# Optimization experiments

Hardware: AMD Instinct MI355X
Metric: run time of the kernel (lower is better)

Reference implementation:

```python
import jax, jax.numpy as jnp
import numpy as np

B, INPLANES, H, W = 32, 1024, 14, 14
PLANES, WIDTH, OUTC = 256, 256, 1024   # width = planes*(base_width/64)*groups; OUTC = planes*4
BITS = (2, 4, 8)                        # bit_list -> lv = 2**bit per expert
GN_GROUPS = 4
EPS = 1e-5


def _qact(x, lv):
    # quantized ReLU (PACT-style, clip [0,1], lv uniform levels) with STE
    y = jnp.clip(x, 0.0, 1.0)
    q = jnp.round(y * (lv - 1)) / (lv - 1)
    return y + jax.lax.stop_gradient(q - y)


def _qw(w, lv):
    # symmetric per-tensor weight quantization with STE
    n = lv // 2 - 1
    if n < 1:
        n = 1
    s = jnp.max(jnp.abs(w)) + 1e-12
    q = jnp.round(w / s * n) / n * s
    return w + jax.lax.stop_gradient(q - w)


def _conv(x, w, stride=1, pad=0):
    return jax.lax.conv_general_dilated(
        x, w, (stride, stride), [(pad, pad), (pad, pad)],
        dimension_numbers=('NCHW', 'OIHW', 'NCHW'))


def _bn(x, g, b, m, v):
    # inference-mode BatchNorm2d with running stats
    inv = g / jnp.sqrt(v + EPS)
    return x * inv[:, None, None] + (b - m * inv)[:, None, None]


def _expert(x, lv, w1, w2, w3, bn1, bn2):
    # quantized Bottleneck expert: qrelu -> conv1x1 -> bn -> relu -> qrelu -> conv3x3 -> bn -> relu -> qrelu -> conv1x1
    h = _conv(_qact(x, lv), _qw(w1, lv))
    h = jax.nn.relu(_bn(h, *bn1))
    h = _conv(_qact(h, lv), _qw(w2, lv), stride=1, pad=1)
    h = jax.nn.relu(_bn(h, *bn2))
    return _conv(_qact(h, lv), _qw(w3, lv))


def setup_inputs() -> dict:
    key = jax.random.key(0)
    ks = jax.random.split(key, 16)
    return {
        'x': jax.random.normal(ks[0], (B, INPLANES, H, W), jnp.float32),
        'mask': jax.random.randint(ks[1], (B,), 0, len(BITS), jnp.int32),
        'w1': jax.random.normal(ks[2], (WIDTH, INPLANES, 1, 1), jnp.float32) * 0.03,
        'w2': jax.random.normal(ks[3], (WIDTH, WIDTH, 3, 3), jnp.float32) * 0.03,
        'w3': jax.random.normal(ks[4], (OUTC, WIDTH, 1, 1), jnp.float32) * 0.03,
        'bn1_g': jax.random.uniform(ks[5], (WIDTH,), jnp.float32, 0.5, 1.5),
        'bn1_b': jax.random.normal(ks[6], (WIDTH,), jnp.float32) * 0.1,
        'bn1_m': jax.random.normal(ks[7], (WIDTH,), jnp.float32) * 0.1,
        'bn1_v': jax.random.uniform(ks[8], (WIDTH,), jnp.float32, 0.5, 1.5),
        'bn2_g': jax.random.uniform(ks[9], (WIDTH,), jnp.float32, 0.5, 1.5),
        'bn2_b': jax.random.normal(ks[10], (WIDTH,), jnp.float32) * 0.1,
        'bn2_m': jax.random.normal(ks[11], (WIDTH,), jnp.float32) * 0.1,
        'bn2_v': jax.random.uniform(ks[12], (WIDTH,), jnp.float32, 0.5, 1.5),
        'gn_g': jax.random.uniform(ks[13], (OUTC,), jnp.float32, 0.5, 1.5),
        'gn_b': jax.random.normal(ks[14], (OUTC,), jnp.float32) * 0.1,
    }


def reference(x, mask, w1, w2, w3, bn1_g, bn1_b, bn1_m, bn1_v,
              bn2_g, bn2_b, bn2_m, bn2_v, gn_g, gn_b):
    bn1 = (bn1_g, bn1_b, bn1_m, bn1_v)
    bn2 = (bn2_g, bn2_b, bn2_m, bn2_v)
    # sparse MoE: per-sample mask selects one quantized expert; combine masked outputs
    out = jnp.zeros((x.shape[0], OUTC, x.shape[2], x.shape[3]), x.dtype)
    for e, bit in enumerate(BITS):
        sel = (mask == e).astype(x.dtype)[:, None, None, None]
        out = out + sel * _expert(x, 2 ** bit, w1, w2, w3, bn1, bn2)
    # GroupNorm(4, OUTC)
    b_, c_, h_, w_ = out.shape
    g = out.reshape(b_, GN_GROUPS, c_ // GN_GROUPS, h_, w_)
    mu = g.mean(axis=(2, 3, 4), keepdims=True)
    var = g.var(axis=(2, 3, 4), keepdims=True)
    g = (g - mu) / jnp.sqrt(var + EPS)
    out = g.reshape(b_, c_, h_, w_) * gn_g[:, None, None] + gn_b[:, None, None]
    # residual (downsample=None, inplanes == planes*expansion) + relu
    return jax.nn.relu(out + x)
```

## Files before the change

kernel.cpp:

```cpp
#include <hip/hip_runtime.h>
#include <hip/hip_bf16.h>

typedef __attribute__((ext_vector_type(8))) short short8;
typedef __attribute__((ext_vector_type(4))) float f32x4;

#define PIX  196
#define EPSN 1e-5f

#define BO_XQ   256
#define BO_W2Q  BO_XQ
#define BO_W3Q  (BO_XQ + 3538944)
#define BO_H1Q  (BO_XQ + 12845056)
#define BO_H2Q  (BO_H1Q + 3211264)
#define BO_W1Q  (BO_H2Q + 3211264)
#define BO_GNS  (BO_W1Q + 1572864)
#define BO_PMAX (BO_GNS + 8192)

__device__ __forceinline__ float e_ascale(int e) { return e == 0 ? 3.f : (e == 1 ? 15.f : 255.f); }
__device__ __forceinline__ float e_nq(int e)     { return e == 0 ? 1.f : (e == 1 ? 7.f : 127.f); }

__device__ __forceinline__ f32x4 mfma16(short8 a, short8 b, f32x4 c) {
    return __builtin_amdgcn_mfma_f32_16x16x32_bf16(a, b, c, 0, 0, 0);
}
__device__ __forceinline__ float wmax_reduce(const char* wsb, int t) {
    const float* pm = (const float*)(wsb + BO_PMAX) + t * 48;
    float s = 0.f;
    #pragma unroll
    for (int k = 0; k < 48; ++k) s = fmaxf(s, pm[k]);
    return s + 1e-12f;
}

__global__ __launch_bounds__(256) void maxabs_kernel(
        const float* __restrict__ w1, const float* __restrict__ w2,
        const float* __restrict__ w3, float* __restrict__ pmax) {
    int t = blockIdx.y;
    const float* w = t == 0 ? w1 : (t == 1 ? w2 : w3);
    int n = (t == 1) ? 256 * 256 * 9 : 256 * 1024;
    float m = 0.f;
    for (int i = blockIdx.x * 256 + threadIdx.x; i < n; i += 48 * 256)
        m = fmaxf(m, fabsf(w[i]));
    __shared__ float red[256];
    red[threadIdx.x] = m;
    __syncthreads();
    for (int s = 128; s > 0; s >>= 1) {
        if (threadIdx.x < s) red[threadIdx.x] = fmaxf(red[threadIdx.x], red[threadIdx.x + s]);
        __syncthreads();
    }
    if (threadIdx.x == 0) pmax[t * 48 + blockIdx.x] = red[0];
}

__global__ __launch_bounds__(256) void prep_w1x(
        const float* __restrict__ w1, const float* __restrict__ x,
        const int* __restrict__ mask, char* wsb) {
    __shared__ float xs[64][197];
    if (blockIdx.x < 1024) {
        int idx = blockIdx.x * 256 + threadIdx.x;
        float s = wmax_reduce(wsb, 0);
        float v = w1[idx];
        __hip_bfloat16* dst = (__hip_bfloat16*)(wsb + BO_W1Q);
        #pragma unroll
        for (int e = 0; e < 3; ++e)
            dst[e * 262144 + idx] = __float2bfloat16(rintf(v / s * e_nq(e)));
    } else {
        int bx = blockIdx.x - 1024;
        int b = bx >> 4, c0 = (bx & 15) * 64;
        float ascale = e_ascale(mask[b]);
        int tid = threadIdx.x;
        for (int idx = tid; idx < 64 * 196; idx += 256) {
            int ci = idx / 196, p = idx - ci * 196;
            xs[ci][p] = x[((size_t)b * 1024 + c0 + ci) * 196 + p];
        }
        __syncthreads();
        __hip_bfloat16* xq = (__hip_bfloat16*)(wsb + BO_XQ);
        for (int idx = tid; idx < 196 * 64; idx += 256) {
            int p = idx / 64, ci = idx - p * 64;
            float v = fminf(fmaxf(xs[ci][p], 0.f), 1.f);
            xq[((size_t)b * 196 + p) * 1024 + c0 + ci] = __float2bfloat16(rintf(v * ascale));
        }
    }
}

__global__ __launch_bounds__(256) void prepw23_kernel(
        const float* __restrict__ w2, const float* __restrict__ w3, char* wsb) {
    int idx = blockIdx.x * 256 + threadIdx.x;
    if (idx < 589824) {
        float s = wmax_reduce(wsb, 1);
        float v = w2[idx];
        int co = idx / 2304, r = idx - co * 2304, ci = r / 9, tap = r - ci * 9;
        __hip_bfloat16* dst = (__hip_bfloat16*)(wsb + BO_W2Q);
        size_t off = ((size_t)tap * 256 + co) * 256 + ci;
        #pragma unroll
        for (int e = 0; e < 3; ++e)
            dst[e * 589824 + off] = __float2bfloat16(rintf(v / s * e_nq(e)));
    } else {
        int i2 = idx - 589824;
        float s = wmax_reduce(wsb, 2);
        float v = w3[i2];
        __hip_bfloat16* dst = (__hip_bfloat16*)(wsb + BO_W3Q);
        #pragma unroll
        for (int e = 0; e < 3; ++e)
            dst[e * 262144 + i2] = __float2bfloat16(rintf(v / s * e_nq(e)));
    }
}

__global__ __launch_bounds__(256) void conv1_mfma(
        char* wsb, const int* __restrict__ mask,
        const float* __restrict__ bg, const float* __restrict__ bb,
        const float* __restrict__ bm, const float* __restrict__ bv) {
    int b = blockIdx.z;
    int e = mask[b];
    float ascale = e_ascale(e);
    float s1 = wmax_reduce(wsb, 0);
    float kscale = (s1 / e_nq(e)) / ascale;

    const short* xq  = (const short*)(wsb + BO_XQ) + (size_t)b * 196 * 1024;
    const short* w1q = (const short*)(wsb + BO_W1Q) + (size_t)e * 256 * 1024;
    __hip_bfloat16* h1q = (__hip_bfloat16*)(wsb + BO_H1Q) + (size_t)b * 196 * 256;

    __shared__ short As[64 * 136];
    __shared__ short Bs[128 * 136];

    int tid = threadIdx.x, w = tid >> 6, lane = tid & 63, r15 = lane & 15, g = lane >> 4;
    int px0 = blockIdx.x * 56, coB = blockIdx.y * 128;

    short8 ra[4], rb[8];
    auto load_tile = [&](int t) {
        int k0 = t * 128;
        #pragma unroll
        for (int ii = 0; ii < 4; ++ii) {
            int idx = ii * 256 + tid;
            int arow = idx >> 4, ac = (idx & 15) * 8;
            ra[ii] = *(const short8*)(xq + (size_t)min(px0 + arow, 195) * 1024 + k0 + ac);
        }
        #pragma unroll
        for (int ii = 0; ii < 8; ++ii) {
            int idx = ii * 256 + tid;
            int brow = idx >> 4, bc = (idx & 15) * 8;
            rb[ii] = *(const short8*)(w1q + (size_t)(coB + brow) * 1024 + k0 + bc);
        }
    };
    auto store_tile = [&]() {
        #pragma unroll
        for (int ii = 0; ii < 4; ++ii) {
            int idx = ii * 256 + tid;
            *(short8*)(As + (idx >> 4) * 136 + (idx & 15) * 8) = ra[ii];
        }
        #pragma unroll
        for (int ii = 0; ii < 8; ++ii) {
            int idx = ii * 256 + tid;
            *(short8*)(Bs + (idx >> 4) * 136 + (idx & 15) * 8) = rb[ii];
        }
    };

    f32x4 acc[4][2] = {};
    load_tile(0);
    for (int t = 0; t < 8; ++t) {
        __syncthreads();
        store_tile();
        __syncthreads();
        if (t < 7) load_tile(t + 1);
        #pragma unroll
        for (int ks = 0; ks < 4; ++ks) {
            short8 bf0 = *(const short8*)(Bs + (w * 32 + r15) * 136 + ks * 32 + g * 8);
            short8 bf1 = *(const short8*)(Bs + (w * 32 + 16 + r15) * 136 + ks * 32 + g * 8);
            #pragma unroll
            for (int m = 0; m < 4; ++m) {
                short8 af = *(const short8*)(As + (m * 16 + r15) * 136 + ks * 32 + g * 8);
                acc[m][0] = mfma16(af, bf0, acc[m][0]);
                acc[m][1] = mfma16(af, bf1, acc[m][1]);
            }
        }
    }
    #pragma unroll
    for (int n = 0; n < 2; ++n) {
        int co = coB + w * 32 + n * 16 + r15;
        float inv = bg[co] * rsqrtf(bv[co] + EPSN);
        float mm = kscale * inv;
        float beta = bb[co] - bm[co] * inv;
        #pragma unroll
        for (int m = 0; m < 4; ++m)
            #pragma unroll
            for (int r = 0; r < 4; ++r) {
                int s = m * 16 + g * 4 + r, px = px0 + s;
                if (s < 56 && px < 196) {
                    float h = fmaxf(acc[m][n][r] * mm + beta, 0.f);
                    h1q[(size_t)px * 256 + co] = __float2bfloat16(rintf(fminf(h, 1.f) * ascale));
                }
            }
    }
}

__global__ __launch_bounds__(256) void conv2_mfma(
        char* wsb, const int* __restrict__ mask,
        const float* __restrict__ bg, const float* __restrict__ bb,
        const float* __restrict__ bm, const float* __restrict__ bv) {
    int b = blockIdx.z;
    int e = mask[b];
    float ascale = e_ascale(e);
    float s2 = wmax_reduce(wsb, 1);
    float kscale = (s2 / e_nq(e)) / ascale;

    const short* h1q = (const short*)(wsb + BO_H1Q) + (size_t)b * 196 * 256;
    const short* w2q = (const short*)(wsb + BO_W2Q) + (size_t)e * 589824;
    __hip_bfloat16* h2q = (__hip_bfloat16*)(wsb + BO_H2Q) + (size_t)b * 196 * 256;

    __shared__ short Xs[6 * 16 * 40];
    __shared__ short Ws9[9 * 64 * 40];

    int tid = threadIdx.x, w = tid >> 6, lane = tid & 63, r15 = lane & 15, g = lane >> 4;
    int r0 = blockIdx.x * 4;
    int px0 = blockIdx.x * 56;
    int coB = blockIdx.y * 64;
    const short8 z8 = {0, 0, 0, 0, 0, 0, 0, 0};

    int wco = tid >> 2, wc8 = (tid & 3) * 8;

    int rr[4], cc[4];
    #pragma unroll
    for (int m = 0; m < 4; ++m) {
        int s0 = min(m * 16 + r15, 55);
        rr[m] = s0 / 14; cc[m] = s0 - rr[m] * 14;
    }

    short8 rx[2], rw[9];
    auto load_tile = [&](int sl) {
        int ci0 = sl * 32;
        #pragma unroll
        for (int ii = 0; ii < 2; ++ii) {
            int idx = ii * 256 + tid;
            rx[ii] = z8;
            if (idx < 384) {
                int xc = idx & 3, xsx = (idx >> 2) & 15, xsy = idx >> 6;
                int iy = r0 - 1 + xsy, ix = xsx - 1;
                if ((unsigned)iy < 14u && (unsigned)ix < 14u)
                    rx[ii] = *(const short8*)(h1q + (size_t)(iy * 14 + ix) * 256 + ci0 + xc * 8);
            }
        }
        #pragma unroll
        for (int tap = 0; tap < 9; ++tap)
            rw[tap] = *(const short8*)(w2q + ((size_t)tap * 256 + coB + wco) * 256 + ci0 + wc8);
    };
    auto store_tile = [&]() {
        #pragma unroll
        for (int ii = 0; ii < 2; ++ii) {
            int idx = ii * 256 + tid;
            if (idx < 384) {
                int xc = idx & 3, xsx = (idx >> 2) & 15, xsy = idx >> 6;
                *(short8*)(Xs + (xsy * 16 + xsx) * 40 + xc * 8) = rx[ii];
            }
        }
        #pragma unroll
        for (int tap = 0; tap < 9; ++tap)
            *(short8*)(Ws9 + (tap * 64 + wco) * 40 + wc8) = rw[tap];
    };

    f32x4 acc[4] = {};
    load_tile(0);
    for (int sl = 0; sl < 8; ++sl) {
        __syncthreads();
        store_tile();
        __syncthreads();
        if (sl < 7) load_tile(sl + 1);
        #pragma unroll
        for (int tap = 0; tap < 9; ++tap) {
            int ty = tap / 3, tx = tap - ty * 3;
            short8 bf = *(const short8*)(Ws9 + (tap * 64 + w * 16 + r15) * 40 + g * 8);
            #pragma unroll
            for (int m = 0; m < 4; ++m) {
                short8 af = *(const short8*)(Xs + ((rr[m] + ty) * 16 + cc[m] + tx) * 40 + g * 8);
                acc[m] = mfma16(af, bf, acc[m]);
            }
        }
    }
    int co = coB + w * 16 + r15;
    float inv = bg[co] * rsqrtf(bv[co] + EPSN);
    float mm = kscale * inv;
    float beta = bb[co] - bm[co] * inv;
    #pragma unroll
    for (int m = 0; m < 4; ++m)
        #pragma unroll
        for (int r = 0; r < 4; ++r) {
            int s = m * 16 + g * 4 + r, px = px0 + s;
            if (s < 56 && px < 196) {
                float h = fmaxf(acc[m][r] * mm + beta, 0.f);
                h2q[(size_t)px * 256 + co] = __float2bfloat16(rintf(fminf(h, 1.f) * ascale));
            }
        }
}

__global__ __launch_bounds__(256) void conv3_mfma(
        char* wsb, const int* __restrict__ mask, float* __restrict__ out) {
    int b = blockIdx.z;
    int e = mask[b];
    float ascale = e_ascale(e);
    float s3 = wmax_reduce(wsb, 2);
    float kscale = (s3 / e_nq(e)) / ascale;

    const short* h2q = (const short*)(wsb + BO_H2Q) + (size_t)b * 196 * 256;
    const short* w3q = (const short*)(wsb + BO_W3Q) + (size_t)e * 1024 * 256;
    float* ob = out + (size_t)b * 1024 * 196;

    __shared__ float Ct[128 * 58];
    __shared__ float rs[256], rss[256];
    short* As = (short*)Ct;
    short* Bs = As + 64 * 72;

    int tid = threadIdx.x, w = tid >> 6, lane = tid & 63, r15 = lane & 15, g = lane >> 4;
    int px0 = blockIdx.x * 56;
    int coQ = blockIdx.y * 128;
    int gslot = (b * 4 + (blockIdx.y >> 1)) * 8 + (blockIdx.y & 1) * 4 + blockIdx.x;

    short8 ra[2], rb[4];
    auto load_tile = [&](int t) {
        int k0 = t * 64;
        #pragma unroll
        for (int ii = 0; ii < 2; ++ii) {
            int idx = ii * 256 + tid;
            int arow = idx >> 3, ac = (idx & 7) * 8;
            ra[ii] = *(const short8*)(h2q + (size_t)min(px0 + arow, 195) * 256 + k0 + ac);
        }
        #pragma unroll
        for (int ii = 0; ii < 4; ++ii) {
            int idx = ii * 256 + tid;
            int brow = idx >> 3, bc = (idx & 7) * 8;
            rb[ii] = *(const short8*)(w3q + (size_t)(coQ + brow) * 256 + k0 + bc);
        }
    };
    auto store_tile = [&]() {
        #pragma unroll
        for (int ii = 0; ii < 2; ++ii) {
            int idx = ii * 256 + tid;
            *(short8*)(As + (idx >> 3) * 72 + (idx & 7) * 8) = ra[ii];
        }
        #pragma unroll
        for (int ii = 0; ii < 4; ++ii) {
            int idx = ii * 256 + tid;
            *(short8*)(Bs + (idx >> 3) * 72 + (idx & 7) * 8) = rb[ii];
        }
    };

    f32x4 acc[4][2] = {};
    load_tile(0);
    for (int t = 0; t < 4; ++t) {
        __syncthreads();
        store_tile();
        __syncthreads();
        if (t < 3) load_tile(t + 1);
        #pragma unroll
        for (int ks = 0; ks < 2; ++ks) {
            short8 bf0 = *(const short8*)(Bs + (w * 32 + r15) * 72 + ks * 32 + g * 8);
            short8 bf1 = *(const short8*)(Bs + (w * 32 + 16 + r15) * 72 + ks * 32 + g * 8);
            #pragma unroll
            for (int m = 0; m < 4; ++m) {
                short8 af = *(const short8*)(As + (m * 16 + r15) * 72 + ks * 32 + g * 8);
                acc[m][0] = mfma16(af, bf0, acc[m][0]);
                acc[m][1] = mfma16(af, bf1, acc[m][1]);
            }
        }
    }
    __syncthreads();
    #pragma unroll
    for (int n = 0; n < 2; ++n)
        #pragma unroll
        for (int m = 0; m < 4; ++m)
            #pragma unroll
            for (int r = 0; r < 4; ++r) {
                int s = m * 16 + g * 4 + r;
                if (s < 56) Ct[(w * 32 + n * 16 + r15) * 58 + s] = acc[m][n][r];
            }
    __syncthreads();
    float sum = 0.f, ss = 0.f;
    for (int idx = tid; idx < 128 * 56; idx += 256) {
        int col = idx / 56, s = idx - col * 56, px = px0 + s;
        if (px < 196) {
            float v = Ct[col * 58 + s] * kscale;
            ob[(size_t)(coQ + col) * 196 + px] = v;
            sum += v; ss += v * v;
        }
    }
    rs[tid] = sum; rss[tid] = ss;
    __syncthreads();
    for (int st = 128; st > 0; st >>= 1) {
        if (tid < st) { rs[tid] += rs[tid + st]; rss[tid] += rss[tid + st]; }
        __syncthreads();
    }
    if (tid == 0) {
        float* gns = (float*)(wsb + BO_GNS);
        gns[gslot * 2] = rs[0];
        gns[gslot * 2 + 1] = rss[0];
    }
}

__global__ __launch_bounds__(256) void gn_apply(
        float* __restrict__ out, const float* __restrict__ x,
        const float* __restrict__ gg, const float* __restrict__ gb, const char* wsb) {
    int bgid = blockIdx.x >> 4, six = blockIdx.x & 15;
    int g = bgid & 3;
    const float* gns = (const float*)(wsb + BO_GNS);
    float s = 0.f, q = 0.f;
    #pragma unroll
    for (int k = 0; k < 8; ++k) { s += gns[(bgid * 8 + k) * 2]; q += gns[(bgid * 8 + k) * 2 + 1]; }
    float mu = s * (1.f / 50176.f);
    float var = q * (1.f / 50176.f) - mu * mu;
    float rstd = rsqrtf(var + EPSN);

    size_t base = (size_t)bgid * 50176 + six * 3136;
    float4* po = (float4*)(out + base);
    const float4* px4 = (const float4*)(x + base);
    int tid = threadIdx.x;
    for (int i = tid; i < 784; i += 256) {
        int off = six * 3136 + i * 4;
        int gc = g * 256 + off / 196;
        float sc = gg[gc] * rstd;
        float sh = gb[gc] - mu * sc;
        float4 v = po[i], xv = px4[i];
        v.x = fmaxf(v.x * sc + sh + xv.x, 0.f);
        v.y = fmaxf(v.y * sc + sh + xv.y, 0.f);
        v.z = fmaxf(v.z * sc + sh + xv.z, 0.f);
        v.w = fmaxf(v.w * sc + sh + xv.w, 0.f);
        po[i] = v;
    }
}

extern "C" void kernel_launch(void* const* d_in, const int* in_sizes, int n_in,
                              void* d_out, int out_size, void* d_ws, size_t ws_size,
                              hipStream_t stream) {
    (void)in_sizes; (void)n_in; (void)out_size; (void)ws_size;
    const float* x    = (const float*)d_in[0];
    const int*   mask = (const int*)d_in[1];
    const float* w1   = (const float*)d_in[2];
    const float* w2   = (const float*)d_in[3];
    const float* w3   = (const float*)d_in[4];
    const float* b1g  = (const float*)d_in[5];
    const float* b1b  = (const float*)d_in[6];
    const float* b1m  = (const float*)d_in[7];
    const float* b1v  = (const float*)d_in[8];
    const float* b2g  = (const float*)d_in[9];
    const float* b2b  = (const float*)d_in[10];
    const float* b2m  = (const float*)d_in[11];
    const float* b2v  = (const float*)d_in[12];
    const float* gng  = (const float*)d_in[13];
    const float* gnb  = (const float*)d_in[14];
    char* wsb = (char*)d_ws;
    float* out = (float*)d_out;

    maxabs_kernel<<<dim3(48, 3), 256, 0, stream>>>(w1, w2, w3, (float*)(wsb + BO_PMAX));
    prep_w1x<<<1536, 256, 0, stream>>>(w1, x, mask, wsb);
    conv1_mfma<<<dim3(4, 2, 32), 256, 0, stream>>>(wsb, mask, b1g, b1b, b1m, b1v);
    prepw23_kernel<<<3328, 256, 0, stream>>>(w2, w3, wsb);
    conv2_mfma<<<dim3(4, 4, 32), 256, 0, stream>>>(wsb, mask, b2g, b2b, b2m, b2v);
    conv3_mfma<<<dim3(4, 8, 32), 256, 0, stream>>>(wsb, mask, out);
    gn_apply<<<2048, 256, 0, stream>>>(out, x, gng, gnb, wsb);
}
```

Before: 101.6 us.

## Quantize w1/w3 on the fly in GEMMs, merge prep kernels, shrink conv tiles

The max-abs reduction now runs inside the same launch as activation quantization, which removes one kernel launch. The separate pre-quantized w1 and w3 buffers are dropped, and conv1 and conv3 now read fp32 weights and quantize them while loading tiles. conv1 and conv2 switch to smaller output tiles (64 and 32 channels) with a 2x2 wave split, which doubles their grid size to raise occupancy and parallelism. The cost is redundant per-block weight quantization and more fp32 weight traffic in the GEMMs, and conv1 now runs twice as many K iterations with smaller tiles.

```diff
diff --git a/kernel.cpp b/kernel.cpp
--- a/kernel.cpp
+++ b/kernel.cpp
@@ -9,11 +9,9 @@
 
 #define BO_XQ   256
 #define BO_W2Q  BO_XQ
-#define BO_W3Q  (BO_XQ + 3538944)
 #define BO_H1Q  (BO_XQ + 12845056)
 #define BO_H2Q  (BO_H1Q + 3211264)
-#define BO_W1Q  (BO_H2Q + 3211264)
-#define BO_GNS  (BO_W1Q + 1572864)
+#define BO_GNS  (BO_H2Q + 3211264 + 1572864)
 #define BO_PMAX (BO_GNS + 8192)
 
 __device__ __forceinline__ float e_ascale(int e) { return e == 0 ? 3.f : (e == 1 ? 15.f : 255.f); }
@@ -29,43 +27,43 @@
     for (int k = 0; k < 48; ++k) s = fmaxf(s, pm[k]);
     return s + 1e-12f;
 }
-
-__global__ __launch_bounds__(256) void maxabs_kernel(
+__device__ __forceinline__ short8 quant8f(const float* p, float qs) {
+    float4 a = *(const float4*)p;
+    float4 b = *(const float4*)(p + 4);
+    float v[8] = {a.x, a.y, a.z, a.w, b.x, b.y, b.z, b.w};
+    short8 r;
+    #pragma unroll
+    for (int j = 0; j < 8; ++j) {
+        __hip_bfloat16 h = __float2bfloat16(rintf(v[j] * qs));
+        r[j] = *reinterpret_cast<short*>(&h);
+    }
+    return r;
+}
+
+__global__ __launch_bounds__(256) void prep0(
         const float* __restrict__ w1, const float* __restrict__ w2,
-        const float* __restrict__ w3, float* __restrict__ pmax) {
-    int t = blockIdx.y;
-    const float* w = t == 0 ? w1 : (t == 1 ? w2 : w3);
-    int n = (t == 1) ? 256 * 256 * 9 : 256 * 1024;
-    float m = 0.f;
-    for (int i = blockIdx.x * 256 + threadIdx.x; i < n; i += 48 * 256)
-        m = fmaxf(m, fabsf(w[i]));
-    __shared__ float red[256];
-    red[threadIdx.x] = m;
-    __syncthreads();
-    for (int s = 128; s > 0; s >>= 1) {
-        if (threadIdx.x < s) red[threadIdx.x] = fmaxf(red[threadIdx.x], red[threadIdx.x + s]);
-        __syncthreads();
-    }
-    if (threadIdx.x == 0) pmax[t * 48 + blockIdx.x] = red[0];
-}
-
-__global__ __launch_bounds__(256) void prep_w1x(
-        const float* __restrict__ w1, const float* __restrict__ x,
+        const float* __restrict__ w3, const float* __restrict__ x,
         const int* __restrict__ mask, char* wsb) {
     __shared__ float xs[64][197];
-    if (blockIdx.x < 1024) {
-        int idx = blockIdx.x * 256 + threadIdx.x;
-        float s = wmax_reduce(wsb, 0);
-        float v = w1[idx];
-        __hip_bfloat16* dst = (__hip_bfloat16*)(wsb + BO_W1Q);
-        #pragma unroll
-        for (int e = 0; e < 3; ++e)
-            dst[e * 262144 + idx] = __float2bfloat16(rintf(v / s * e_nq(e)));
+    int tid = threadIdx.x;
+    if (blockIdx.x < 144) {
+        int t = blockIdx.x / 48, j = blockIdx.x - t * 48;
+        const float* w = t == 0 ? w1 : (t == 1 ? w2 : w3);
+        int n = (t == 1) ? 256 * 256 * 9 : 256 * 1024;
+        float m = 0.f;
+        for (int i = j * 256 + tid; i < n; i += 48 * 256) m = fmaxf(m, fabsf(w[i]));
+        float* red = &xs[0][0];
+        red[tid] = m;
+        __syncthreads();
+        for (int s = 128; s > 0; s >>= 1) {
+            if (tid < s) red[tid] = fmaxf(red[tid], red[tid + s]);
+            __syncthreads();
+        }
+        if (tid == 0) ((float*)(wsb + BO_PMAX))[t * 48 + j] = red[0];
     } else {
-        int bx = blockIdx.x - 1024;
+        int bx = blockIdx.x - 144;
         int b = bx >> 4, c0 = (bx & 15) * 64;
         float ascale = e_ascale(mask[b]);
-        int tid = threadIdx.x;
         for (int idx = tid; idx < 64 * 196; idx += 256) {
             int ci = idx / 196, p = idx - ci * 196;
             xs[ci][p] = x[((size_t)b * 1024 + c0 + ci) * 196 + p];
@@ -80,92 +78,74 @@
     }
 }
 
-__global__ __launch_bounds__(256) void prepw23_kernel(
-        const float* __restrict__ w2, const float* __restrict__ w3, char* wsb) {
+__global__ __launch_bounds__(256) void prepw2_kernel(const float* __restrict__ w2, char* wsb) {
     int idx = blockIdx.x * 256 + threadIdx.x;
-    if (idx < 589824) {
-        float s = wmax_reduce(wsb, 1);
-        float v = w2[idx];
-        int co = idx / 2304, r = idx - co * 2304, ci = r / 9, tap = r - ci * 9;
-        __hip_bfloat16* dst = (__hip_bfloat16*)(wsb + BO_W2Q);
-        size_t off = ((size_t)tap * 256 + co) * 256 + ci;
-        #pragma unroll
-        for (int e = 0; e < 3; ++e)
-            dst[e * 589824 + off] = __float2bfloat16(rintf(v / s * e_nq(e)));
-    } else {
-        int i2 = idx - 589824;
-        float s = wmax_reduce(wsb, 2);
-        float v = w3[i2];
-        __hip_bfloat16* dst = (__hip_bfloat16*)(wsb + BO_W3Q);
-        #pragma unroll
-        for (int e = 0; e < 3; ++e)
-            dst[e * 262144 + i2] = __float2bfloat16(rintf(v / s * e_nq(e)));
-    }
+    float s = wmax_reduce(wsb, 1);
+    float v = w2[idx];
+    int co = idx / 2304, r = idx - co * 2304, ci = r / 9, tap = r - ci * 9;
+    __hip_bfloat16* dst = (__hip_bfloat16*)(wsb + BO_W2Q);
+    size_t off = ((size_t)tap * 256 + co) * 256 + ci;
+    #pragma unroll
+    for (int e = 0; e < 3; ++e)
+        dst[e * 589824 + off] = __float2bfloat16(rintf(v / s * e_nq(e)));
 }
 
 __global__ __launch_bounds__(256) void conv1_mfma(
-        char* wsb, const int* __restrict__ mask,
+        char* wsb, const int* __restrict__ mask, const float* __restrict__ w1,
         const float* __restrict__ bg, const float* __restrict__ bb,
         const float* __restrict__ bm, const float* __restrict__ bv) {
     int b = blockIdx.z;
     int e = mask[b];
-    float ascale = e_ascale(e);
+    float ascale = e_ascale(e), nq = e_nq(e);
     float s1 = wmax_reduce(wsb, 0);
-    float kscale = (s1 / e_nq(e)) / ascale;
-
-    const short* xq  = (const short*)(wsb + BO_XQ) + (size_t)b * 196 * 1024;
-    const short* w1q = (const short*)(wsb + BO_W1Q) + (size_t)e * 256 * 1024;
+    float qs = nq / s1;
+    float kscale = (s1 / nq) / ascale;
+
+    const short* xq = (const short*)(wsb + BO_XQ) + (size_t)b * 196 * 1024;
     __hip_bfloat16* h1q = (__hip_bfloat16*)(wsb + BO_H1Q) + (size_t)b * 196 * 256;
 
-    __shared__ short As[64 * 136];
-    __shared__ short Bs[128 * 136];
+    __shared__ short As[64 * 72];
+    __shared__ short Bs[64 * 72];
 
     int tid = threadIdx.x, w = tid >> 6, lane = tid & 63, r15 = lane & 15, g = lane >> 4;
-    int px0 = blockIdx.x * 56, coB = blockIdx.y * 128;
-
-    short8 ra[4], rb[8];
+    int mh = w >> 1, nh = w & 1;
+    int px0 = blockIdx.x * 56, coB = blockIdx.y * 64;
+
+    short8 ra[2], rb[2];
     auto load_tile = [&](int t) {
-        int k0 = t * 128;
-        #pragma unroll
-        for (int ii = 0; ii < 4; ++ii) {
-            int idx = ii * 256 + tid;
-            int arow = idx >> 4, ac = (idx & 15) * 8;
-            ra[ii] = *(const short8*)(xq + (size_t)min(px0 + arow, 195) * 1024 + k0 + ac);
-        }
-        #pragma unroll
-        for (int ii = 0; ii < 8; ++ii) {
-            int idx = ii * 256 + tid;
-            int brow = idx >> 4, bc = (idx & 15) * 8;
-            rb[ii] = *(const short8*)(w1q + (size_t)(coB + brow) * 1024 + k0 + bc);
+        int k0 = t * 64;
+        #pragma unroll
+        for (int ii = 0; ii < 2; ++ii) {
+            int idx = ii * 256 + tid;
+            int row = idx >> 3, c8 = (idx & 7) * 8;
+            ra[ii] = *(const short8*)(xq + (size_t)min(px0 + row, 195) * 1024 + k0 + c8);
+            rb[ii] = quant8f(w1 + (size_t)(coB + row) * 1024 + k0 + c8, qs);
         }
     };
     auto store_tile = [&]() {
         #pragma unroll
-        for (int ii = 0; ii < 4; ++ii) {
-            int idx = ii * 256 + tid;
-            *(short8*)(As + (idx >> 4) * 136 + (idx & 15) * 8) = ra[ii];
-        }
-        #pragma unroll
-        for (int ii = 0; ii < 8; ++ii) {
-            int idx = ii * 256 + tid;
-            *(short8*)(Bs + (idx >> 4) * 136 + (idx & 15) * 8) = rb[ii];
-        }
-    };
-
-    f32x4 acc[4][2] = {};
+        for (int ii = 0; ii < 2; ++ii) {
+            int idx = ii * 256 + tid;
+            int row = idx >> 3, c8 = (idx & 7) * 8;
+            *(short8*)(As + row * 72 + c8) = ra[ii];
+            *(short8*)(Bs + row * 72 + c8) = rb[ii];
+        }
+    };
+
+    f32x4 acc[2][2] = {};
     load_tile(0);
-    for (int t = 0; t < 8; ++t) {
+    for (int t = 0; t < 16; ++t) {
         __syncthreads();
         store_tile();
         __syncthreads();
-        if (t < 7) load_tile(t + 1);
-        #pragma unroll
-        for (int ks = 0; ks < 4; ++ks) {
-            short8 bf0 = *(const short8*)(Bs + (w * 32 + r15) * 136 + ks * 32 + g * 8);
-            short8 bf1 = *(const short8*)(Bs + (w * 32 + 16 + r15) * 136 + ks * 32 + g * 8);
+        if (t < 15) load_tile(t + 1);
+        #pragma unroll
+        for (int ks = 0; ks < 2; ++ks) {
+            short8 bf0 = *(const short8*)(Bs + (nh * 32 + r15) * 72 + ks * 32 + g * 8);
+            short8 bf1 = *(const short8*)(Bs + (nh * 32 + 16 + r15) * 72 + ks * 32 + g * 8);
             #pragma unroll
-            for (int m = 0; m < 4; ++m) {
-                short8 af = *(const short8*)(As + (m * 16 + r15) * 136 + ks * 32 + g * 8);
+            for (int m = 0; m < 2; ++m) {
+                short8 af = *(const short8*)(As + (mh * 32 + m * 16 + r15) * 72 + ks * 32 + g * 8);
                 acc[m][0] = mfma16(af, bf0, acc[m][0]);
                 acc[m][1] = mfma16(af, bf1, acc[m][1]);
             }
@@ -173,15 +153,15 @@
     }
     #pragma unroll
     for (int n = 0; n < 2; ++n) {
-        int co = coB + w * 32 + n * 16 + r15;
+        int co = coB + nh * 32 + n * 16 + r15;
         float inv = bg[co] * rsqrtf(bv[co] + EPSN);
         float mm = kscale * inv;
         float beta = bb[co] - bm[co] * inv;
         #pragma unroll
-        for (int m = 0; m < 4; ++m)
+        for (int m = 0; m < 2; ++m)
             #pragma unroll
             for (int r = 0; r < 4; ++r) {
-                int s = m * 16 + g * 4 + r, px = px0 + s;
+                int s = mh * 32 + m * 16 + g * 4 + r, px = px0 + s;
                 if (s < 56 && px < 196) {
                     float h = fmaxf(acc[m][n][r] * mm + beta, 0.f);
                     h1q[(size_t)px * 256 + co] = __float2bfloat16(rintf(fminf(h, 1.f) * ascale));
@@ -204,25 +184,24 @@
     const short* w2q = (const short*)(wsb + BO_W2Q) + (size_t)e * 589824;
     __hip_bfloat16* h2q = (__hip_bfloat16*)(wsb + BO_H2Q) + (size_t)b * 196 * 256;
 
-    __shared__ short Xs[6 * 16 * 40];
-    __shared__ short Ws9[9 * 64 * 40];
+    __shared__ short Xs[6 * 16 * 34];
+    __shared__ short Ws9[9 * 32 * 34];
 
     int tid = threadIdx.x, w = tid >> 6, lane = tid & 63, r15 = lane & 15, g = lane >> 4;
+    int mh = w >> 1, nh = w & 1;
     int r0 = blockIdx.x * 4;
     int px0 = blockIdx.x * 56;
-    int coB = blockIdx.y * 64;
+    int coB = blockIdx.y * 32;
     const short8 z8 = {0, 0, 0, 0, 0, 0, 0, 0};
 
-    int wco = tid >> 2, wc8 = (tid & 3) * 8;
-
-    int rr[4], cc[4];
-    #pragma unroll
-    for (int m = 0; m < 4; ++m) {
-        int s0 = min(m * 16 + r15, 55);
+    int rr[2], cc[2];
+    #pragma unroll
+    for (int m = 0; m < 2; ++m) {
+        int s0 = min(mh * 32 + m * 16 + r15, 55);
         rr[m] = s0 / 14; cc[m] = s0 - rr[m] * 14;
     }
 
-    short8 rx[2], rw[9];
+    short8 rx[2], rw[5];
     auto load_tile = [&](int sl) {
         int ci0 = sl * 32;
         #pragma unroll
@@ -237,8 +216,13 @@
             }
         }
         #pragma unroll
-        for (int tap = 0; tap < 9; ++tap)
-            rw[tap] = *(const short8*)(w2q + ((size_t)tap * 256 + coB + wco) * 256 + ci0 + wc8);
+        for (int ii = 0; ii < 5; ++ii) {
+            int idx = ii * 256 + tid;
+            if (idx < 1152) {
+                int tap = idx >> 7, rem = idx & 127, co = rem >> 2, c8 = (rem & 3) * 8;
+                rw[ii] = *(const short8*)(w2q + ((size_t)tap * 256 + coB + co) * 256 + ci0 + c8);
+            }
+        }
     };
     auto store_tile = [&]() {
         #pragma unroll
@@ -246,15 +230,20 @@
             int idx = ii * 256 + tid;
             if (idx < 384) {
                 int xc = idx & 3, xsx = (idx >> 2) & 15, xsy = idx >> 6;
-                *(short8*)(Xs + (xsy * 16 + xsx) * 40 + xc * 8) = rx[ii];
-            }
-        }
-        #pragma unroll
-        for (int tap = 0; tap < 9; ++tap)
-            *(short8*)(Ws9 + (tap * 64 + wco) * 40 + wc8) = rw[tap];
-    };
-
-    f32x4 acc[4] = {};
+                *(short8*)(Xs + (xsy * 16 + xsx) * 34 + xc * 8) = rx[ii];
+            }
+        }
+        #pragma unroll
+        for (int ii = 0; ii < 5; ++ii) {
+            int idx = ii * 256 + tid;
+            if (idx < 1152) {
+                int tap = idx >> 7, rem = idx & 127, co = rem >> 2, c8 = (rem & 3) * 8;
+                *(short8*)(Ws9 + (tap * 32 + co) * 34 + c8) = rw[ii];
+            }
+        }
+    };
+
+    f32x4 acc[2] = {};
     load_tile(0);
     for (int sl = 0; sl < 8; ++sl) {
         __syncthreads();
@@ -264,23 +253,23 @@
         #pragma unroll
         for (int tap = 0; tap < 9; ++tap) {
             int ty = tap / 3, tx = tap - ty * 3;
-            short8 bf = *(const short8*)(Ws9 + (tap * 64 + w * 16 + r15) * 40 + g * 8);
+            short8 bf = *(const short8*)(Ws9 + (tap * 32 + nh * 16 + r15) * 34 + g * 8);
             #pragma unroll
-            for (int m = 0; m < 4; ++m) {
-                short8 af = *(const short8*)(Xs + ((rr[m] + ty) * 16 + cc[m] + tx) * 40 + g * 8);
+            for (int m = 0; m < 2; ++m) {
+                short8 af = *(const short8*)(Xs + ((rr[m] + ty) * 16 + cc[m] + tx) * 34 + g * 8);
                 acc[m] = mfma16(af, bf, acc[m]);
             }
         }
     }
-    int co = coB + w * 16 + r15;
+    int co = coB + nh * 16 + r15;
     float inv = bg[co] * rsqrtf(bv[co] + EPSN);
     float mm = kscale * inv;
     float beta = bb[co] - bm[co] * inv;
     #pragma unroll
-    for (int m = 0; m < 4; ++m)
+    for (int m = 0; m < 2; ++m)
         #pragma unroll
         for (int r = 0; r < 4; ++r) {
-            int s = m * 16 + g * 4 + r, px = px0 + s;
+            int s = mh * 32 + m * 16 + g * 4 + r, px = px0 + s;
             if (s < 56 && px < 196) {
                 float h = fmaxf(acc[m][r] * mm + beta, 0.f);
                 h2q[(size_t)px * 256 + co] = __float2bfloat16(rintf(fminf(h, 1.f) * ascale));
@@ -289,15 +278,16 @@
 }
 
 __global__ __launch_bounds__(256) void conv3_mfma(
-        char* wsb, const int* __restrict__ mask, float* __restrict__ out) {
+        char* wsb, const int* __restrict__ mask, const float* __restrict__ w3,
+        float* __restrict__ out) {
     int b = blockIdx.z;
     int e = mask[b];
-    float ascale = e_ascale(e);
+    float ascale = e_ascale(e), nq = e_nq(e);
     float s3 = wmax_reduce(wsb, 2);
-    float kscale = (s3 / e_nq(e)) / ascale;
+    float qs = nq / s3;
+    float kscale = (s3 / nq) / ascale;
 
     const short* h2q = (const short*)(wsb + BO_H2Q) + (size_t)b * 196 * 256;
-    const short* w3q = (const short*)(wsb + BO_W3Q) + (size_t)e * 1024 * 256;
     float* ob = out + (size_t)b * 1024 * 196;
 
     __shared__ float Ct[128 * 58];
@@ -323,7 +313,7 @@
         for (int ii = 0; ii < 4; ++ii) {
             int idx = ii * 256 + tid;
             int brow = idx >> 3, bc = (idx & 7) * 8;
-            rb[ii] = *(const short8*)(w3q + (size_t)(coQ + brow) * 256 + k0 + bc);
+            rb[ii] = quant8f(w3 + (size_t)(coQ + brow) * 256 + k0 + bc, qs);
         }
     };
     auto store_tile = [&]() {
@@ -444,11 +434,10 @@
     char* wsb = (char*)d_ws;
     float* out = (float*)d_out;
 
-    maxabs_kernel<<<dim3(48, 3), 256, 0, stream>>>(w1, w2, w3, (float*)(wsb + BO_PMAX));
-    prep_w1x<<<1536, 256, 0, stream>>>(w1, x, mask, wsb);
-    conv1_mfma<<<dim3(4, 2, 32), 256, 0, stream>>>(wsb, mask, b1g, b1b, b1m, b1v);
-    prepw23_kernel<<<3328, 256, 0, stream>>>(w2, w3, wsb);
-    conv2_mfma<<<dim3(4, 4, 32), 256, 0, stream>>>(wsb, mask, b2g, b2b, b2m, b2v);
-    conv3_mfma<<<dim3(4, 8, 32), 256, 0, stream>>>(wsb, mask, out);
+    prep0<<<656, 256, 0, stream>>>(w1, w2, w3, x, mask, wsb);
+    conv1_mfma<<<dim3(4, 4, 32), 256, 0, stream>>>(wsb, mask, w1, b1g, b1b, b1m, b1v);
+    prepw2_kernel<<<2304, 256, 0, stream>>>(w2, wsb);
+    conv2_mfma<<<dim3(4, 8, 32), 256, 0, stream>>>(wsb, mask, b2g, b2b, b2m, b2v);
+    conv3_mfma<<<dim3(4, 8, 32), 256, 0, stream>>>(wsb, mask, w3, out);
     gn_apply<<<2048, 256, 0, stream>>>(out, x, gng, gnb, wsb);
 }
```

Result: slower. 107.2 us (+5.5%).

## Merge prep kernels, retile conv1, stage conv3 output as bf16 in workspace

Applied to the files above, without the earlier changes.

Merges the w1/x and w2/w3 quantization kernels into a single prep_all launch. Quantized w2/w3 now live in the output buffer, and conv3 writes its pre-norm result as bf16 into the freed xq region. conv1 moves to a 64x64 tile with K=64 steps, which gives twice as many blocks and uses less LDS. gn_apply then reads half as many bytes for the intermediate, at the cost of rounding it to bf16 before GroupNorm, which adds numeric error.

```diff
diff --git a/kernel.cpp b/kernel.cpp
--- a/kernel.cpp
+++ b/kernel.cpp
@@ -8,13 +8,13 @@
 #define EPSN 1e-5f
 
 #define BO_XQ   256
-#define BO_W2Q  BO_XQ
-#define BO_W3Q  (BO_XQ + 3538944)
 #define BO_H1Q  (BO_XQ + 12845056)
 #define BO_H2Q  (BO_H1Q + 3211264)
 #define BO_W1Q  (BO_H2Q + 3211264)
 #define BO_GNS  (BO_W1Q + 1572864)
 #define BO_PMAX (BO_GNS + 8192)
+#define DO_W2Q  0
+#define DO_W3Q  3538944
 
 __device__ __forceinline__ float e_ascale(int e) { return e == 0 ? 3.f : (e == 1 ? 15.f : 255.f); }
 __device__ __forceinline__ float e_nq(int e)     { return e == 0 ? 1.f : (e == 1 ? 7.f : 127.f); }
@@ -29,16 +29,19 @@
     for (int k = 0; k < 48; ++k) s = fmaxf(s, pm[k]);
     return s + 1e-12f;
 }
+__device__ __forceinline__ float bf16s_to_f32(short h) {
+    unsigned u = ((unsigned)(unsigned short)h) << 16;
+    return __uint_as_float(u);
+}
 
 __global__ __launch_bounds__(256) void maxabs_kernel(
         const float* __restrict__ w1, const float* __restrict__ w2,
         const float* __restrict__ w3, float* __restrict__ pmax) {
-    int t = blockIdx.y;
+    int t = blockIdx.x / 48, j = blockIdx.x - t * 48;
     const float* w = t == 0 ? w1 : (t == 1 ? w2 : w3);
     int n = (t == 1) ? 256 * 256 * 9 : 256 * 1024;
     float m = 0.f;
-    for (int i = blockIdx.x * 256 + threadIdx.x; i < n; i += 48 * 256)
-        m = fmaxf(m, fabsf(w[i]));
+    for (int i = j * 256 + threadIdx.x; i < n; i += 48 * 256) m = fmaxf(m, fabsf(w[i]));
     __shared__ float red[256];
     red[threadIdx.x] = m;
     __syncthreads();
@@ -46,26 +49,18 @@
         if (threadIdx.x < s) red[threadIdx.x] = fmaxf(red[threadIdx.x], red[threadIdx.x + s]);
         __syncthreads();
     }
-    if (threadIdx.x == 0) pmax[t * 48 + blockIdx.x] = red[0];
-}
-
-__global__ __launch_bounds__(256) void prep_w1x(
-        const float* __restrict__ w1, const float* __restrict__ x,
-        const int* __restrict__ mask, char* wsb) {
+    if (threadIdx.x == 0) pmax[t * 48 + j] = red[0];
+}
+
+__global__ __launch_bounds__(256) void prep_all(
+        const float* __restrict__ w1, const float* __restrict__ w2,
+        const float* __restrict__ w3, const float* __restrict__ x,
+        const int* __restrict__ mask, char* wsb, char* doutb) {
     __shared__ float xs[64][197];
-    if (blockIdx.x < 1024) {
-        int idx = blockIdx.x * 256 + threadIdx.x;
-        float s = wmax_reduce(wsb, 0);
-        float v = w1[idx];
-        __hip_bfloat16* dst = (__hip_bfloat16*)(wsb + BO_W1Q);
-        #pragma unroll
-        for (int e = 0; e < 3; ++e)
-            dst[e * 262144 + idx] = __float2bfloat16(rintf(v / s * e_nq(e)));
-    } else {
-        int bx = blockIdx.x - 1024;
+    int tid = threadIdx.x, bx = blockIdx.x;
+    if (bx < 512) {
         int b = bx >> 4, c0 = (bx & 15) * 64;
         float ascale = e_ascale(mask[b]);
-        int tid = threadIdx.x;
         for (int idx = tid; idx < 64 * 196; idx += 256) {
             int ci = idx / 196, p = idx - ci * 196;
             xs[ci][p] = x[((size_t)b * 1024 + c0 + ci) * 196 + p];
@@ -77,29 +72,32 @@
             float v = fminf(fmaxf(xs[ci][p], 0.f), 1.f);
             xq[((size_t)b * 196 + p) * 1024 + c0 + ci] = __float2bfloat16(rintf(v * ascale));
         }
-    }
-}
-
-__global__ __launch_bounds__(256) void prepw23_kernel(
-        const float* __restrict__ w2, const float* __restrict__ w3, char* wsb) {
-    int idx = blockIdx.x * 256 + threadIdx.x;
-    if (idx < 589824) {
+    } else if (bx < 1536) {
+        int idx = (bx - 512) * 256 + tid;
+        float s = wmax_reduce(wsb, 0);
+        float v = w1[idx];
+        __hip_bfloat16* dst = (__hip_bfloat16*)(wsb + BO_W1Q);
+        #pragma unroll
+        for (int e = 0; e < 3; ++e)
+            dst[e * 262144 + idx] = __float2bfloat16(rintf(v / s * e_nq(e)));
+    } else if (bx < 3840) {
+        int idx = (bx - 1536) * 256 + tid;
         float s = wmax_reduce(wsb, 1);
         float v = w2[idx];
         int co = idx / 2304, r = idx - co * 2304, ci = r / 9, tap = r - ci * 9;
-        __hip_bfloat16* dst = (__hip_bfloat16*)(wsb + BO_W2Q);
+        __hip_bfloat16* dst = (__hip_bfloat16*)(doutb + DO_W2Q);
         size_t off = ((size_t)tap * 256 + co) * 256 + ci;
         #pragma unroll
         for (int e = 0; e < 3; ++e)
             dst[e * 589824 + off] = __float2bfloat16(rintf(v / s * e_nq(e)));
     } else {
-        int i2 = idx - 589824;
+        int idx = (bx - 3840) * 256 + tid;
         float s = wmax_reduce(wsb, 2);
-        float v = w3[i2];
-        __hip_bfloat16* dst = (__hip_bfloat16*)(wsb + BO_W3Q);
+        float v = w3[idx];
+        __hip_bfloat16* dst = (__hip_bfloat16*)(doutb + DO_W3Q);
         #pragma unroll
         for (int e = 0; e < 3; ++e)
-            dst[e * 262144 + i2] = __float2bfloat16(rintf(v / s * e_nq(e)));
+            dst[e * 262144 + idx] = __float2bfloat16(rintf(v / s * e_nq(e)));
     }
 }
 
@@ -114,58 +112,51 @@
     float kscale = (s1 / e_nq(e)) / ascale;
 
     const short* xq  = (const short*)(wsb + BO_XQ) + (size_t)b * 196 * 1024;
-    const short* w1q = (const short*)(wsb + BO_W1Q) + (size_t)e * 256 * 1024;
+    const short* w1q = (const short*)(wsb + BO_W1Q) + (size_t)e * 262144;
     __hip_bfloat16* h1q = (__hip_bfloat16*)(wsb + BO_H1Q) + (size_t)b * 196 * 256;
 
-    __shared__ short As[64 * 136];
-    __shared__ short Bs[128 * 136];
+    __shared__ short As[64 * 72];
+    __shared__ short Bs[64 * 72];
 
     int tid = threadIdx.x, w = tid >> 6, lane = tid & 63, r15 = lane & 15, g = lane >> 4;
-    int px0 = blockIdx.x * 56, coB = blockIdx.y * 128;
-
-    short8 ra[4], rb[8];
+    int mh = w >> 1, nh = w & 1;
+    int px0 = blockIdx.x * 56, coB = blockIdx.y * 64;
+
+    short8 ra[2], rb[2];
     auto load_tile = [&](int t) {
-        int k0 = t * 128;
-        #pragma unroll
-        for (int ii = 0; ii < 4; ++ii) {
-            int idx = ii * 256 + tid;
-            int arow = idx >> 4, ac = (idx & 15) * 8;
-            ra[ii] = *(const short8*)(xq + (size_t)min(px0 + arow, 195) * 1024 + k0 + ac);
-        }
-        #pragma unroll
-        for (int ii = 0; ii < 8; ++ii) {
-            int idx = ii * 256 + tid;
-            int brow = idx >> 4, bc = (idx & 15) * 8;
-            rb[ii] = *(const short8*)(w1q + (size_t)(coB + brow) * 1024 + k0 + bc);
+        int k0 = t * 64;
+        #pragma unroll
+        for (int ii = 0; ii < 2; ++ii) {
+            int idx = ii * 256 + tid;
+            int row = idx >> 3, c8 = (idx & 7) * 8;
+            ra[ii] = *(const short8*)(xq + (size_t)min(px0 + row, 195) * 1024 + k0 + c8);
+            rb[ii] = *(const short8*)(w1q + (size_t)(coB + row) * 1024 + k0 + c8);
         }
     };
     auto store_tile = [&]() {
         #pragma unroll
-        for (int ii = 0; ii < 4; ++ii) {
-            int idx = ii * 256 + tid;
-            *(short8*)(As + (idx >> 4) * 136 + (idx & 15) * 8) = ra[ii];
-        }
-        #pragma unroll
-        for (int ii = 0; ii < 8; ++ii) {
-            int idx = ii * 256 + tid;
-            *(short8*)(Bs + (idx >> 4) * 136 + (idx & 15) * 8) = rb[ii];
-        }
-    };
-
-    f32x4 acc[4][2] = {};
+        for (int ii = 0; ii < 2; ++ii) {
+            int idx = ii * 256 + tid;
+            int row = idx >> 3, c8 = (idx & 7) * 8;
+            *(short8*)(As + row * 72 + c8) = ra[ii];
+            *(short8*)(Bs + row * 72 + c8) = rb[ii];
+        }
+    };
+
+    f32x4 acc[2][2] = {};
     load_tile(0);
-    for (int t = 0; t < 8; ++t) {
+    for (int t = 0; t < 16; ++t) {
         __syncthreads();
         store_tile();
         __syncthreads();
-        if (t < 7) load_tile(t + 1);
-        #pragma unroll
-        for (int ks = 0; ks < 4; ++ks) {
-            short8 bf0 = *(const short8*)(Bs + (w * 32 + r15) * 136 + ks * 32 + g * 8);
-            short8 bf1 = *(const short8*)(Bs + (w * 32 + 16 + r15) * 136 + ks * 32 + g * 8);
+        if (t < 15) load_tile(t + 1);
+        #pragma unroll
+        for (int ks = 0; ks < 2; ++ks) {
+            short8 bf0 = *(const short8*)(Bs + (nh * 32 + r15) * 72 + ks * 32 + g * 8);
+            short8 bf1 = *(const short8*)(Bs + (nh * 32 + 16 + r15) * 72 + ks * 32 + g * 8);
             #pragma unroll
-            for (int m = 0; m < 4; ++m) {
-                short8 af = *(const short8*)(As + (m * 16 + r15) * 136 + ks * 32 + g * 8);
+            for (int m = 0; m < 2; ++m) {
+                short8 af = *(const short8*)(As + (mh * 32 + m * 16 + r15) * 72 + ks * 32 + g * 8);
                 acc[m][0] = mfma16(af, bf0, acc[m][0]);
                 acc[m][1] = mfma16(af, bf1, acc[m][1]);
             }
@@ -173,15 +164,15 @@
     }
     #pragma unroll
     for (int n = 0; n < 2; ++n) {
-        int co = coB + w * 32 + n * 16 + r15;
+        int co = coB + nh * 32 + n * 16 + r15;
         float inv = bg[co] * rsqrtf(bv[co] + EPSN);
         float mm = kscale * inv;
         float beta = bb[co] - bm[co] * inv;
         #pragma unroll
-        for (int m = 0; m < 4; ++m)
+        for (int m = 0; m < 2; ++m)
             #pragma unroll
             for (int r = 0; r < 4; ++r) {
-                int s = m * 16 + g * 4 + r, px = px0 + s;
+                int s = mh * 32 + m * 16 + g * 4 + r, px = px0 + s;
                 if (s < 56 && px < 196) {
                     float h = fmaxf(acc[m][n][r] * mm + beta, 0.f);
                     h1q[(size_t)px * 256 + co] = __float2bfloat16(rintf(fminf(h, 1.f) * ascale));
@@ -191,7 +182,7 @@
 }
 
 __global__ __launch_bounds__(256) void conv2_mfma(
-        char* wsb, const int* __restrict__ mask,
+        char* wsb, const char* __restrict__ doutb, const int* __restrict__ mask,
         const float* __restrict__ bg, const float* __restrict__ bb,
         const float* __restrict__ bm, const float* __restrict__ bv) {
     int b = blockIdx.z;
@@ -201,7 +192,7 @@
     float kscale = (s2 / e_nq(e)) / ascale;
 
     const short* h1q = (const short*)(wsb + BO_H1Q) + (size_t)b * 196 * 256;
-    const short* w2q = (const short*)(wsb + BO_W2Q) + (size_t)e * 589824;
+    const short* w2q = (const short*)(doutb + DO_W2Q) + (size_t)e * 589824;
     __hip_bfloat16* h2q = (__hip_bfloat16*)(wsb + BO_H2Q) + (size_t)b * 196 * 256;
 
     __shared__ short Xs[6 * 16 * 40];
@@ -289,7 +280,7 @@
 }
 
 __global__ __launch_bounds__(256) void conv3_mfma(
-        char* wsb, const int* __restrict__ mask, float* __restrict__ out) {
+        char* wsb, const char* __restrict__ doutb, const int* __restrict__ mask) {
     int b = blockIdx.z;
     int e = mask[b];
     float ascale = e_ascale(e);
@@ -297,8 +288,8 @@
     float kscale = (s3 / e_nq(e)) / ascale;
 
     const short* h2q = (const short*)(wsb + BO_H2Q) + (size_t)b * 196 * 256;
-    const short* w3q = (const short*)(wsb + BO_W3Q) + (size_t)e * 1024 * 256;
-    float* ob = out + (size_t)b * 1024 * 196;
+    const short* w3q = (const short*)(doutb + DO_W3Q) + (size_t)e * 262144;
+    __hip_bfloat16* pg = (__hip_bfloat16*)(wsb + BO_XQ) + (size_t)b * 1024 * 196;
 
     __shared__ float Ct[128 * 58];
     __shared__ float rs[256], rss[256];
@@ -374,8 +365,10 @@
         int col = idx / 56, s = idx - col * 56, px = px0 + s;
         if (px < 196) {
             float v = Ct[col * 58 + s] * kscale;
-            ob[(size_t)(coQ + col) * 196 + px] = v;
-            sum += v; ss += v * v;
+            __hip_bfloat16 hv = __float2bfloat16(v);
+            float vq = __bfloat162float(hv);
+            pg[(size_t)(coQ + col) * 196 + px] = hv;
+            sum += vq; ss += vq * vq;
         }
     }
     rs[tid] = sum; rss[tid] = ss;
@@ -392,33 +385,43 @@
 }
 
 __global__ __launch_bounds__(256) void gn_apply(
-        float* __restrict__ out, const float* __restrict__ x,
-        const float* __restrict__ gg, const float* __restrict__ gb, const char* wsb) {
+        const char* __restrict__ wsb, const float* __restrict__ x,
+        const float* __restrict__ gg, const float* __restrict__ gb,
+        float* __restrict__ out) {
     int bgid = blockIdx.x >> 4, six = blockIdx.x & 15;
     int g = bgid & 3;
     const float* gns = (const float*)(wsb + BO_GNS);
-    float s = 0.f, q = 0.f;
-    #pragma unroll
-    for (int k = 0; k < 8; ++k) { s += gns[(bgid * 8 + k) * 2]; q += gns[(bgid * 8 + k) * 2 + 1]; }
-    float mu = s * (1.f / 50176.f);
-    float var = q * (1.f / 50176.f) - mu * mu;
+    float S = 0.f, Q = 0.f;
+    #pragma unroll
+    for (int k = 0; k < 8; ++k) { S += gns[(bgid * 8 + k) * 2]; Q += gns[(bgid * 8 + k) * 2 + 1]; }
+    float mu = S * (1.f / 50176.f);
+    float var = Q * (1.f / 50176.f) - mu * mu;
     float rstd = rsqrtf(var + EPSN);
 
-    size_t base = (size_t)bgid * 50176 + six * 3136;
-    float4* po = (float4*)(out + base);
-    const float4* px4 = (const float4*)(x + base);
+    const __hip_bfloat16* pg = (const __hip_bfloat16*)(wsb + BO_XQ) + (size_t)bgid * 50176;
+    const float* xg = x + (size_t)bgid * 50176;
+    float* og = out + (size_t)bgid * 50176;
+
     int tid = threadIdx.x;
-    for (int i = tid; i < 784; i += 256) {
-        int off = six * 3136 + i * 4;
-        int gc = g * 256 + off / 196;
-        float sc = gg[gc] * rstd;
-        float sh = gb[gc] - mu * sc;
-        float4 v = po[i], xv = px4[i];
-        v.x = fmaxf(v.x * sc + sh + xv.x, 0.f);
-        v.y = fmaxf(v.y * sc + sh + xv.y, 0.f);
-        v.z = fmaxf(v.z * sc + sh + xv.z, 0.f);
-        v.w = fmaxf(v.w * sc + sh + xv.w, 0.f);
-        po[i] = v;
+    for (int i = tid; i < 392; i += 256) {
+        int eb = six * 3136 + i * 8;
+        int c = eb / 196, r = eb - c * 196;
+        short8 hv = *(const short8*)(pg + eb);
+        float4 x0 = *(const float4*)(xg + eb);
+        float4 x1 = *(const float4*)(xg + eb + 4);
+        float xv[8] = {x0.x, x0.y, x0.z, x0.w, x1.x, x1.y, x1.z, x1.w};
+        float o[8];
+        #pragma unroll
+        for (int j = 0; j < 8; ++j) {
+            int gc = g * 256 + c;
+            float sc = gg[gc] * rstd;
+            float sh = gb[gc] - mu * sc;
+            float v = bf16s_to_f32(hv[j]);
+            o[j] = fmaxf(v * sc + sh + xv[j], 0.f);
+            if (++r == 196) { r = 0; ++c; }
+        }
+        *(float4*)(og + eb)     = make_float4(o[0], o[1], o[2], o[3]);
+        *(float4*)(og + eb + 4) = make_float4(o[4], o[5], o[6], o[7]);
     }
 }
 
@@ -442,13 +445,13 @@
     const float* gng  = (const float*)d_in[13];
     const float* gnb  = (const float*)d_in[14];
     char* wsb = (char*)d_ws;
+    char* doutb = (char*)d_out;
     float* out = (float*)d_out;
 
-    maxabs_kernel<<<dim3(48, 3), 256, 0, stream>>>(w1, w2, w3, (float*)(wsb + BO_PMAX));
-    prep_w1x<<<1536, 256, 0, stream>>>(w1, x, mask, wsb);
-    conv1_mfma<<<dim3(4, 2, 32), 256, 0, stream>>>(wsb, mask, b1g, b1b, b1m, b1v);
-    prepw23_kernel<<<3328, 256, 0, stream>>>(w2, w3, wsb);
-    conv2_mfma<<<dim3(4, 4, 32), 256, 0, stream>>>(wsb, mask, b2g, b2b, b2m, b2v);
-    conv3_mfma<<<dim3(4, 8, 32), 256, 0, stream>>>(wsb, mask, out);
-    gn_apply<<<2048, 256, 0, stream>>>(out, x, gng, gnb, wsb);
-}
+    maxabs_kernel<<<144, 256, 0, stream>>>(w1, w2, w3, (float*)(wsb + BO_PMAX));
+    prep_all<<<4864, 256, 0, stream>>>(w1, w2, w3, x, mask, wsb, doutb);
+    conv1_mfma<<<dim3(4, 4, 32), 256, 0, stream>>>(wsb, mask, b1g, b1b, b1m, b1v);
+    conv2_mfma<<<dim3(4, 4, 32), 256, 0, stream>>>(wsb, doutb, mask, b2g, b2b, b2m, b2v);
+    conv3_mfma<<<dim3(4, 8, 32), 256, 0, stream>>>(wsb, doutb, mask);
+    gn_apply<<<2048, 256, 0, stream>>>(wsb, x, gng, gnb, out);
+}
```

Result: faster. 92.16 us (-9.3%).
